# Kernel tuning notes

Measured on AMD Instinct MI355X. Metric: run time of the kernel, lower is better.

The kernel has to match this reference:

```python
import jax, jax.numpy as jnp
import numpy as np

N = 8192
F_IN = 128
N_META = 128
N_EMBED = 128


def setup_inputs() -> dict:
    key = jax.random.key(0)
    k1, k2, k3, k4, k5, k6 = jax.random.split(key, 6)
    X = jax.random.normal(k1, (N, F_IN), dtype=jnp.float32)
    A = jax.random.uniform(k2, (N, N), dtype=jnp.float32)  # dense nonneg adjacency
    s = 1.0 / np.sqrt(F_IN)
    W_embed = jax.random.uniform(k3, (N_EMBED, F_IN), dtype=jnp.float32, minval=-s, maxval=s)
    b_embed = jax.random.uniform(k4, (N_EMBED,), dtype=jnp.float32, minval=-s, maxval=s)
    W_assign = jax.random.uniform(k5, (N_META, F_IN), dtype=jnp.float32, minval=-s, maxval=s)
    b_assign = jax.random.uniform(k6, (N_META,), dtype=jnp.float32, minval=-s, maxval=s)
    return {"X": X, "A": A, "W_embed": W_embed, "b_embed": b_embed,
            "W_assign": W_assign, "b_assign": b_assign}


def reference(X, A, W_embed, b_embed, W_assign, b_assign):
    n = A.shape[0]
    # A_hat = A + I; symmetric normalization D^-1/2 A_hat D^-1/2.
    # (Original builds full diag matrices; result equals row/col scaling.)
    A_hat = A + jnp.eye(n, dtype=A.dtype)
    deg = jnp.sum(A_hat, axis=1)
    d_inv_sqrt = jnp.where(deg > 0, jax.lax.rsqrt(deg), 0.0)
    A_norm = d_inv_sqrt[:, None] * A_hat * d_inv_sqrt[None, :]
    AX = A_norm @ X  # shared by both GCN layers: [N, F]
    z_l = AX @ W_embed.T + b_embed                      # [N, n_embed]
    s_l = jax.nn.softmax(AX @ W_assign.T + b_assign, axis=-1)  # [N, n_meta]
    X_next = s_l.T @ z_l                                 # [n_meta, n_embed]
    A_next = s_l.T @ (A @ s_l)                           # [n_meta, n_meta]
    return (X_next, A_next, s_l)
```

## Files before the change

### kernel.cpp

```cpp
#include <hip/hip_runtime.h>
#include <hip/hip_bf16.h>
#include <cstdint>

typedef short v8s __attribute__((ext_vector_type(8)));
typedef float v4f __attribute__((ext_vector_type(4)));

#define DEV __device__ __forceinline__

DEV unsigned short f2bu(float f) {
  unsigned u = __builtin_bit_cast(unsigned, f);
  u += 0x7fffu + ((u >> 16) & 1u);
  return (unsigned short)(u >> 16);
}

DEV v8s pack8(const float4& a, const float4& b) {
  v8s r;
  r[0] = (short)f2bu(a.x); r[1] = (short)f2bu(a.y);
  r[2] = (short)f2bu(a.z); r[3] = (short)f2bu(a.w);
  r[4] = (short)f2bu(b.x); r[5] = (short)f2bu(b.y);
  r[6] = (short)f2bu(b.z); r[7] = (short)f2bu(b.w);
  return r;
}

DEV void gload16(const unsigned short* g, char* l) {
  __builtin_amdgcn_global_load_lds(
      (const __attribute__((address_space(1))) void*)g,
      (__attribute__((address_space(3))) void*)l, 16, 0, 0);
}

template<bool CVT>
__global__ __launch_bounds__(256)
void k_degcvt(const float* __restrict__ A, float* __restrict__ dinv,
              unsigned short* __restrict__ Abf) {
  const int row = blockIdx.x;
  const float* ar = A + (size_t)row * 8192;
  unsigned short* aw = Abf + (size_t)row * 8192;
  float s = 0.f;
  #pragma unroll
  for (int i = 0; i < 8; ++i) {
    const int c = i * 1024 + threadIdx.x * 4;
    float4 v = *(const float4*)(ar + c);
    s += (v.x + v.y) + (v.z + v.w);
    if constexpr (CVT) {
      uint2 w;
      w.x = (unsigned)f2bu(v.x) | ((unsigned)f2bu(v.y) << 16);
      w.y = (unsigned)f2bu(v.z) | ((unsigned)f2bu(v.w) << 16);
      *(uint2*)(aw + c) = w;
    }
  }
  #pragma unroll
  for (int d = 1; d < 64; d <<= 1) s += __shfl_xor(s, d);
  __shared__ float wsum[4];
  if ((threadIdx.x & 63) == 0) wsum[threadIdx.x >> 6] = s;
  __syncthreads();
  if (threadIdx.x == 0) {
    dinv[row] = rsqrtf(1.0f + ((wsum[0] + wsum[1]) + (wsum[2] + wsum[3])));
  }
}

template<bool SCALE>
__global__ __launch_bounds__(256)
void k_transpose(const float* __restrict__ in, unsigned short* __restrict__ out,
                 const float* __restrict__ dinv) {
  __shared__ float tile[32][129];
  const int j0 = blockIdx.x * 32;
  const int t = threadIdx.x;
  const int r0 = t >> 5, sl = t & 31;
  #pragma unroll
  for (int i = 0; i < 4; ++i) {
    int r = r0 + i * 8;
    float4 v = *(const float4*)(in + (size_t)(j0 + r) * 128 + sl * 4);
    float sc = 1.0f;
    if constexpr (SCALE) sc = dinv[j0 + r];
    tile[r][sl * 4 + 0] = v.x * sc;
    tile[r][sl * 4 + 1] = v.y * sc;
    tile[r][sl * 4 + 2] = v.z * sc;
    tile[r][sl * 4 + 3] = v.w * sc;
  }
  __syncthreads();
  const int c = t >> 1, h = t & 1;
  unsigned short* op = out + (size_t)c * 8192 + j0 + h * 16;
  #pragma unroll
  for (int q = 0; q < 2; ++q) {
    int rb = h * 16 + q * 8;
    uint4 w;
    w.x = (unsigned)f2bu(tile[rb + 0][c]) | ((unsigned)f2bu(tile[rb + 1][c]) << 16);
    w.y = (unsigned)f2bu(tile[rb + 2][c]) | ((unsigned)f2bu(tile[rb + 3][c]) << 16);
    w.z = (unsigned)f2bu(tile[rb + 4][c]) | ((unsigned)f2bu(tile[rb + 5][c]) << 16);
    w.w = (unsigned)f2bu(tile[rb + 6][c]) | ((unsigned)f2bu(tile[rb + 7][c]) << 16);
    *(uint4*)(op + q * 8) = w;
  }
}

__global__ __launch_bounds__(256, 4)
void k_gemm_v2(const unsigned short* __restrict__ Ab16,
               const unsigned short* __restrict__ Bt,
               float* __restrict__ parts) {
  __shared__ alignas(16) char bsm[2][16384];
  const int t = threadIdx.x;
  const int wv = t >> 6, l = t & 63;
  const int wr = wv >> 1, wcol = wv & 1;
  const int i0 = blockIdx.x * 64 + wr * 32;
  const int k0 = blockIdx.y * 1024;
  const int lr = l & 15, lq = l >> 4;

  const unsigned short* pA0 = Ab16 + (size_t)(i0 + lr) * 8192 + k0 + lq * 8;
  const unsigned short* pA1 = pA0 + (size_t)16 * 8192;

  const int swz = (l & 7) ^ ((l >> 3) & 7);
  const unsigned short* pS[4];
  #pragma unroll
  for (int i = 0; i < 4; ++i) {
    const int col = wv * 32 + i * 8 + (l >> 3);
    pS[i] = Bt + (size_t)col * 8192 + k0 + swz * 8;
  }

  v4f acc[2][4];
  #pragma unroll
  for (int mt = 0; mt < 2; ++mt)
    #pragma unroll
    for (int nt = 0; nt < 4; ++nt) acc[mt][nt] = (v4f){0.f, 0.f, 0.f, 0.f};

  v8s areg[2][2][2];

  auto stage = [&](int c, int buf) {
    #pragma unroll
    for (int i = 0; i < 4; ++i)
      gload16(pS[i] + c * 64, bsm[buf] + wv * 4096 + i * 1024);
  };
  auto loadA = [&](int c, int buf) {
    #pragma unroll
    for (int kf = 0; kf < 2; ++kf) {
      areg[buf][kf][0] = *(const v8s*)(pA0 + c * 64 + kf * 32);
      areg[buf][kf][1] = *(const v8s*)(pA1 + c * 64 + kf * 32);
    }
  };

  stage(0, 0);
  loadA(0, 0);
  __syncthreads();

  #pragma unroll
  for (int c = 0; c < 16; ++c) {
    if (c < 15) {
      stage(c + 1, (c + 1) & 1);
      loadA(c + 1, (c + 1) & 1);
    }
    #pragma unroll
    for (int kf = 0; kf < 2; ++kf) {
      #pragma unroll
      for (int nt = 0; nt < 4; ++nt) {
        const int col = wcol * 64 + nt * 16 + lr;
        const int off = ((col << 7) + kf * 64 + lq * 16) ^ ((col & 7) << 4);
        v8s bf = *(const v8s*)(bsm[c & 1] + off);
        acc[0][nt] = __builtin_amdgcn_mfma_f32_16x16x32_bf16(areg[c & 1][kf][0], bf, acc[0][nt], 0, 0, 0);
        acc[1][nt] = __builtin_amdgcn_mfma_f32_16x16x32_bf16(areg[c & 1][kf][1], bf, acc[1][nt], 0, 0, 0);
      }
    }
    if (c < 15) __syncthreads();
  }

  float* p = parts + (size_t)blockIdx.y * (8192 * 128);
  const int colb = wcol * 64;
  #pragma unroll
  for (int mt = 0; mt < 2; ++mt)
    #pragma unroll
    for (int nt = 0; nt < 4; ++nt)
      #pragma unroll
      for (int r = 0; r < 4; ++r)
        p[(size_t)(i0 + mt * 16 + lq * 4 + r) * 128 + colb + nt * 16 + lr] = acc[mt][nt][r];
}

__global__ __launch_bounds__(512)
void k_gemm_f32(const float* __restrict__ Af, const unsigned short* __restrict__ Bt,
                float* __restrict__ parts) {
  constexpr int KSTEPS = 2048 / 32;
  const int t = threadIdx.x;
  const int wv = t >> 6, l = t & 63;
  const int rg = wv >> 1, ch = wv & 1;
  const int i0 = blockIdx.x * 128 + rg * 32;
  const int k0 = blockIdx.y * 2048;
  const int lr = l & 15, lk = (l >> 4) * 8;

  const float* pAf0 = Af + (size_t)(i0 + lr) * 8192 + k0 + lk;
  const float* pAf1 = pAf0 + (size_t)16 * 8192;
  const unsigned short* pB[4];
  #pragma unroll
  for (int nt = 0; nt < 4; ++nt)
    pB[nt] = Bt + (size_t)(ch * 64 + nt * 16 + lr) * 8192 + k0 + lk;

  v4f acc[2][4];
  #pragma unroll
  for (int mt = 0; mt < 2; ++mt)
    #pragma unroll
    for (int nt = 0; nt < 4; ++nt) acc[mt][nt] = (v4f){0.f, 0.f, 0.f, 0.f};

  float4 af_[2][2][2];
  v8s bb[2][4];

  auto loadab = [&](int buf, int k) {
    af_[buf][0][0] = *(const float4*)(pAf0 + k);
    af_[buf][0][1] = *(const float4*)(pAf0 + k + 4);
    af_[buf][1][0] = *(const float4*)(pAf1 + k);
    af_[buf][1][1] = *(const float4*)(pAf1 + k + 4);
    #pragma unroll
    for (int nt = 0; nt < 4; ++nt) bb[buf][nt] = *(const v8s*)(pB[nt] + k);
  };
  auto mfmas = [&](int buf) {
    #pragma unroll
    for (int mt = 0; mt < 2; ++mt) {
      v8s a_ = pack8(af_[buf][mt][0], af_[buf][mt][1]);
      #pragma unroll
      for (int nt = 0; nt < 4; ++nt)
        acc[mt][nt] = __builtin_amdgcn_mfma_f32_16x16x32_bf16(a_, bb[buf][nt], acc[mt][nt], 0, 0, 0);
    }
  };

  loadab(0, 0);
  for (int kt = 0; kt < KSTEPS; kt += 2) {
    loadab(1, (kt + 1) * 32);
    mfmas(0);
    if (kt + 2 < KSTEPS) loadab(0, (kt + 2) * 32);
    mfmas(1);
  }

  float* p = parts + (size_t)blockIdx.y * (8192 * 128);
  const int colb = ch * 64;
  #pragma unroll
  for (int mt = 0; mt < 2; ++mt)
    #pragma unroll
    for (int nt = 0; nt < 4; ++nt)
      #pragma unroll
      for (int r = 0; r < 4; ++r)
        p[(size_t)(i0 + mt * 16 + (l >> 4) * 4 + r) * 128 + colb + nt * 16 + lr] = acc[mt][nt][r];
}

__global__ __launch_bounds__(256)
void k_post1(const float* __restrict__ parts, int nsplit,
             const float* __restrict__ dinv, const float* __restrict__ Xg,
             const float* __restrict__ We, const float* __restrict__ be,
             const float* __restrict__ Wa, const float* __restrict__ ba,
             float* __restrict__ sl_out, unsigned short* __restrict__ slt,
             unsigned short* __restrict__ zlt) {
  __shared__ alignas(16) unsigned short axs[32 * 128];
  __shared__ float lg[32 * 128];
  __shared__ unsigned short sbf[32 * 130];
  __shared__ unsigned short zbf[32 * 130];
  const int t = threadIdx.x;
  const int i0 = blockIdx.x * 32;

  {
    const int r = t >> 3, cg = t & 7;
    const size_t base = (size_t)(i0 + r) * 128 + cg * 16;
    float acc[16];
    #pragma unroll
    for (int q = 0; q < 4; ++q) {
      float4 v = *(const float4*)(parts + base + q * 4);
      acc[q * 4 + 0] = v.x; acc[q * 4 + 1] = v.y;
      acc[q * 4 + 2] = v.z; acc[q * 4 + 3] = v.w;
    }
    for (int s = 1; s < nsplit; ++s) {
      #pragma unroll
      for (int q = 0; q < 4; ++q) {
        float4 v = *(const float4*)(parts + (size_t)s * 1048576 + base + q * 4);
        acc[q * 4 + 0] += v.x; acc[q * 4 + 1] += v.y;
        acc[q * 4 + 2] += v.z; acc[q * 4 + 3] += v.w;
      }
    }
    const float di = dinv[i0 + r];
    unsigned short bx[16];
    #pragma unroll
    for (int q = 0; q < 4; ++q) {
      float4 xv = *(const float4*)(Xg + base + q * 4);
      bx[q * 4 + 0] = f2bu(di * (acc[q * 4 + 0] + di * xv.x));
      bx[q * 4 + 1] = f2bu(di * (acc[q * 4 + 1] + di * xv.y));
      bx[q * 4 + 2] = f2bu(di * (acc[q * 4 + 2] + di * xv.z));
      bx[q * 4 + 3] = f2bu(di * (acc[q * 4 + 3] + di * xv.w));
    }
    char* Ab = (char*)axs;
    const int b0 = (r << 8) + cg * 32, sw = (r & 7) << 4;
    uint4 w0, w1;
    w0.x = (unsigned)bx[0] | ((unsigned)bx[1] << 16);
    w0.y = (unsigned)bx[2] | ((unsigned)bx[3] << 16);
    w0.z = (unsigned)bx[4] | ((unsigned)bx[5] << 16);
    w0.w = (unsigned)bx[6] | ((unsigned)bx[7] << 16);
    w1.x = (unsigned)bx[8] | ((unsigned)bx[9] << 16);
    w1.y = (unsigned)bx[10] | ((unsigned)bx[11] << 16);
    w1.z = (unsigned)bx[12] | ((unsigned)bx[13] << 16);
    w1.w = (unsigned)bx[14] | ((unsigned)bx[15] << 16);
    *(uint4*)(Ab + (b0 ^ sw)) = w0;
    *(uint4*)(Ab + ((b0 + 16) ^ sw)) = w1;
  }
  __syncthreads();

  const int wv = t >> 6, l = t & 63, fr = l & 15;
  {
    v4f zac[2][2], lac[2][2];
    #pragma unroll
    for (int a = 0; a < 2; ++a)
      #pragma unroll
      for (int b = 0; b < 2; ++b) {
        zac[a][b] = (v4f){0.f, 0.f, 0.f, 0.f};
        lac[a][b] = (v4f){0.f, 0.f, 0.f, 0.f};
      }
    const int kk = (l >> 4) * 8;
    #pragma unroll
    for (int ks = 0; ks < 4; ++ks) {
      const int k = ks * 32 + kk;
      #pragma unroll
      for (int nj = 0; nj < 2; ++nj) {
        const int col = nj * 64 + wv * 16 + fr;
        v8s bfe = pack8(*(const float4*)(We + col * 128 + k),
                        *(const float4*)(We + col * 128 + k + 4));
        v8s bfa = pack8(*(const float4*)(Wa + col * 128 + k),
                        *(const float4*)(Wa + col * 128 + k + 4));
        #pragma unroll
        for (int mt = 0; mt < 2; ++mt) {
          const int arow = mt * 16 + fr;
          v8s af = *(const v8s*)((char*)axs + (((arow << 8) + k * 2) ^ ((fr & 7) << 4)));
          zac[mt][nj] = __builtin_amdgcn_mfma_f32_16x16x32_bf16(af, bfe, zac[mt][nj], 0, 0, 0);
          lac[mt][nj] = __builtin_amdgcn_mfma_f32_16x16x32_bf16(af, bfa, lac[mt][nj], 0, 0, 0);
        }
      }
    }
    #pragma unroll
    for (int mt = 0; mt < 2; ++mt)
      #pragma unroll
      for (int nj = 0; nj < 2; ++nj)
        #pragma unroll
        for (int r4 = 0; r4 < 4; ++r4) {
          const int row = mt * 16 + (l >> 4) * 4 + r4;
          const int col = nj * 64 + wv * 16 + fr;
          lg[row * 128 + col] = lac[mt][nj][r4] + ba[col];
          zbf[row * 130 + col] = f2bu(zac[mt][nj][r4] + be[col]);
        }
  }
  __syncthreads();

  {
    const int r = t >> 3, g = t & 7;
    const float* lp = lg + r * 128 + g * 16;
    float x[16];
    #pragma unroll
    for (int q = 0; q < 4; ++q) {
      float4 v = *(const float4*)(lp + q * 4);
      x[q * 4 + 0] = v.x; x[q * 4 + 1] = v.y; x[q * 4 + 2] = v.z; x[q * 4 + 3] = v.w;
    }
    float mx = x[0];
    #pragma unroll
    for (int j = 1; j < 16; ++j) mx = fmaxf(mx, x[j]);
    #pragma unroll
    for (int d = 1; d < 8; d <<= 1) mx = fmaxf(mx, __shfl_xor(mx, d));
    float sum = 0.f;
    #pragma unroll
    for (int j = 0; j < 16; ++j) { x[j] = __expf(x[j] - mx); sum += x[j]; }
    #pragma unroll
    for (int d = 1; d < 8; d <<= 1) sum += __shfl_xor(sum, d);
    const float inv = 1.0f / sum;
    float* op = sl_out + (size_t)(i0 + r) * 128 + g * 16;
    #pragma unroll
    for (int q = 0; q < 4; ++q) {
      float4 o;
      o.x = x[q * 4 + 0] * inv; o.y = x[q * 4 + 1] * inv;
      o.z = x[q * 4 + 2] * inv; o.w = x[q * 4 + 3] * inv;
      *(float4*)(op + q * 4) = o;
    }
    #pragma unroll
    for (int j = 0; j < 16; ++j) sbf[r * 130 + g * 16 + j] = f2bu(x[j] * inv);
  }
  __syncthreads();

  {
    const int c = t & 127;
    const unsigned short* src = (t < 128) ? sbf : zbf;
    unsigned short* dst = (t < 128) ? slt : zlt;
    unsigned short* o = dst + (size_t)c * 8192 + i0;
    #pragma unroll
    for (int q = 0; q < 4; ++q) {
      uint4 w;
      w.x = (unsigned)src[(q * 8 + 0) * 130 + c] | ((unsigned)src[(q * 8 + 1) * 130 + c] << 16);
      w.y = (unsigned)src[(q * 8 + 2) * 130 + c] | ((unsigned)src[(q * 8 + 3) * 130 + c] << 16);
      w.z = (unsigned)src[(q * 8 + 4) * 130 + c] | ((unsigned)src[(q * 8 + 5) * 130 + c] << 16);
      w.w = (unsigned)src[(q * 8 + 6) * 130 + c] | ((unsigned)src[(q * 8 + 7) * 130 + c] << 16);
      *(uint4*)(o + q * 8) = w;
    }
  }
}

__global__ __launch_bounds__(256)
void k_post2(const float* __restrict__ parts, int nsplit, unsigned short* __restrict__ ast) {
  __shared__ unsigned short sb[32 * 130];
  const int t = threadIdx.x;
  const int i0 = blockIdx.x * 32;
  {
    const int r = t >> 3, cg = t & 7;
    const size_t base = (size_t)(i0 + r) * 128 + cg * 16;
    float acc[16];
    #pragma unroll
    for (int q = 0; q < 4; ++q) {
      float4 v = *(const float4*)(parts + base + q * 4);
      acc[q * 4 + 0] = v.x; acc[q * 4 + 1] = v.y;
      acc[q * 4 + 2] = v.z; acc[q * 4 + 3] = v.w;
    }
    for (int s = 1; s < nsplit; ++s) {
      #pragma unroll
      for (int q = 0; q < 4; ++q) {
        float4 v = *(const float4*)(parts + (size_t)s * 1048576 + base + q * 4);
        acc[q * 4 + 0] += v.x; acc[q * 4 + 1] += v.y;
        acc[q * 4 + 2] += v.z; acc[q * 4 + 3] += v.w;
      }
    }
    #pragma unroll
    for (int j = 0; j < 16; ++j) sb[r * 130 + cg * 16 + j] = f2bu(acc[j]);
  }
  __syncthreads();
  if (t < 128) {
    unsigned short* o = ast + (size_t)t * 8192 + i0;
    #pragma unroll
    for (int q = 0; q < 4; ++q) {
      uint4 w;
      w.x = (unsigned)sb[(q * 8 + 0) * 130 + t] | ((unsigned)sb[(q * 8 + 1) * 130 + t] << 16);
      w.y = (unsigned)sb[(q * 8 + 2) * 130 + t] | ((unsigned)sb[(q * 8 + 3) * 130 + t] << 16);
      w.z = (unsigned)sb[(q * 8 + 4) * 130 + t] | ((unsigned)sb[(q * 8 + 5) * 130 + t] << 16);
      w.w = (unsigned)sb[(q * 8 + 6) * 130 + t] | ((unsigned)sb[(q * 8 + 7) * 130 + t] << 16);
      *(uint4*)(o + q * 8) = w;
    }
  }
}

__global__ __launch_bounds__(256)
void k_outer(const unsigned short* __restrict__ slt, const unsigned short* __restrict__ zlt,
             const unsigned short* __restrict__ ast, float* __restrict__ parts) {
  const int t = threadIdx.x, wv = t >> 6, ln = t & 63;
  const int k0 = blockIdx.x * 128;
  const int lm = ln & 15, lk = (ln >> 4) << 3;
  v4f c1[2][8];
  v4f c2[2][8];
  #pragma unroll
  for (int mt = 0; mt < 2; ++mt)
    #pragma unroll
    for (int nt = 0; nt < 8; ++nt) { c1[mt][nt] = (v4f){0.f,0.f,0.f,0.f}; c2[mt][nt] = (v4f){0.f,0.f,0.f,0.f}; }
  #pragma unroll
  for (int ks = 0; ks < 4; ++ks) {
    int k = k0 + ks * 32 + lk;
    v8s a0 = *(const v8s*)(slt + (size_t)(wv * 32 + lm) * 8192 + k);
    v8s a1 = *(const v8s*)(slt + (size_t)(wv * 32 + 16 + lm) * 8192 + k);
    #pragma unroll
    for (int nt = 0; nt < 8; ++nt) {
      v8s bz = *(const v8s*)(zlt + (size_t)(nt * 16 + lm) * 8192 + k);
      v8s bs = *(const v8s*)(ast + (size_t)(nt * 16 + lm) * 8192 + k);
      c1[0][nt] = __builtin_amdgcn_mfma_f32_16x16x32_bf16(a0, bz, c1[0][nt], 0, 0, 0);
      c1[1][nt] = __builtin_amdgcn_mfma_f32_16x16x32_bf16(a1, bz, c1[1][nt], 0, 0, 0);
      c2[0][nt] = __builtin_amdgcn_mfma_f32_16x16x32_bf16(a0, bs, c2[0][nt], 0, 0, 0);
      c2[1][nt] = __builtin_amdgcn_mfma_f32_16x16x32_bf16(a1, bs, c2[1][nt], 0, 0, 0);
    }
  }
  float* p = parts + (size_t)blockIdx.x * 32768;
  #pragma unroll
  for (int mt = 0; mt < 2; ++mt)
    #pragma unroll
    for (int nt = 0; nt < 8; ++nt)
      #pragma unroll
      for (int r = 0; r < 4; ++r) {
        int m = wv * 32 + mt * 16 + ((ln >> 4) << 2) + r;
        int n = nt * 16 + lm;
        p[m * 128 + n] = c1[mt][nt][r];
        p[16384 + m * 128 + n] = c2[mt][nt][r];
      }
}

__global__ __launch_bounds__(256)
void k_reduce(const float* __restrict__ parts, float* __restrict__ out) {
  const int o = blockIdx.x * 256 + threadIdx.x;
  float s = 0.f;
  for (int b = 0; b < 64; ++b) s += parts[(size_t)b * 32768 + o];
  out[o] = s;
}

extern "C" void kernel_launch(void* const* d_in, const int* in_sizes, int n_in,
                              void* d_out, int out_size, void* d_ws, size_t ws_size,
                              hipStream_t stream) {
  (void)in_sizes; (void)n_in; (void)out_size;
  const float* X  = (const float*)d_in[0];
  const float* A  = (const float*)d_in[1];
  const float* We = (const float*)d_in[2];
  const float* be = (const float*)d_in[3];
  const float* Wa = (const float*)d_in[4];
  const float* ba = (const float*)d_in[5];
  float* out = (float*)d_out;
  float* sl = out + 32768;

  char* ws = (char*)d_ws;
  constexpr size_t OFF_XPT  = 32768;
  constexpr size_t OFF_SLT  = OFF_XPT + 2097152;
  constexpr size_t OFF_ZLT  = OFF_SLT + 2097152;
  constexpr size_t OFF_AST  = OFF_ZLT + 2097152;
  constexpr size_t OFF_PART = OFF_AST + 2097152;
  constexpr size_t OFF_ABF  = OFF_PART + 67108864;
  constexpr size_t NEED_ABF = OFF_ABF + 134217728ull;

  float*          dinv = (float*)(ws + 0);
  unsigned short* xpt  = (unsigned short*)(ws + OFF_XPT);
  unsigned short* slt  = (unsigned short*)(ws + OFF_SLT);
  unsigned short* zlt  = (unsigned short*)(ws + OFF_ZLT);
  unsigned short* ast  = (unsigned short*)(ws + OFF_AST);
  float*          part = (float*)(ws + OFF_PART);
  unsigned short* abfp = (unsigned short*)(ws + OFF_ABF);

  const bool abf = ws_size >= NEED_ABF;
  const int  sk  = abf ? 8 : 4;

  if (abf) k_degcvt<true><<<8192, 256, 0, stream>>>(A, dinv, abfp);
  else     k_degcvt<false><<<8192, 256, 0, stream>>>(A, dinv, abfp);

  k_transpose<true><<<256, 256, 0, stream>>>(X, xpt, dinv);

  if (abf) k_gemm_v2<<<dim3(128, 8), 256, 0, stream>>>(abfp, xpt, part);
  else     k_gemm_f32<<<dim3(64, 4), 512, 0, stream>>>(A, xpt, part);

  k_post1<<<256, 256, 0, stream>>>(part, sk, dinv, X, We, be, Wa, ba, sl, slt, zlt);

  if (abf) k_gemm_v2<<<dim3(128, 8), 256, 0, stream>>>(abfp, slt, part);
  else     k_gemm_f32<<<dim3(64, 4), 512, 0, stream>>>(A, slt, part);

  k_post2<<<256, 256, 0, stream>>>(part, sk, ast);
  k_outer<<<64, 256, 0, stream>>>(slt, zlt, ast, part);
  k_reduce<<<128, 256, 0, stream>>>(part, out);
}
```

Measured before the change: 219.4 us.

## Read fp32 A directly in GEMMs and drop the bf16 copy of A

Removes the pre-pass that wrote a bf16 copy of the 8192x8192 adjacency matrix. The LDS-staged GEMM now loads fp32 A rows directly and converts them to bf16 in registers before each MFMA, using a per-k-fragment double-buffered register prefetch. This removes the 128MB bf16 write and the workspace-size fallback path. In exchange, each of the two GEMM passes reads twice as many A bytes, and the conversion arithmetic now sits in the inner loop.

```diff
diff --git a/kernel.cpp b/kernel.cpp
--- a/kernel.cpp
+++ b/kernel.cpp
@@ -28,25 +28,15 @@
       (__attribute__((address_space(3))) void*)l, 16, 0, 0);
 }
 
-template<bool CVT>
-__global__ __launch_bounds__(256)
-void k_degcvt(const float* __restrict__ A, float* __restrict__ dinv,
-              unsigned short* __restrict__ Abf) {
+__global__ __launch_bounds__(256)
+void k_deg(const float* __restrict__ A, float* __restrict__ dinv) {
   const int row = blockIdx.x;
   const float* ar = A + (size_t)row * 8192;
-  unsigned short* aw = Abf + (size_t)row * 8192;
   float s = 0.f;
   #pragma unroll
   for (int i = 0; i < 8; ++i) {
-    const int c = i * 1024 + threadIdx.x * 4;
-    float4 v = *(const float4*)(ar + c);
+    float4 v = *(const float4*)(ar + i * 1024 + threadIdx.x * 4);
     s += (v.x + v.y) + (v.z + v.w);
-    if constexpr (CVT) {
-      uint2 w;
-      w.x = (unsigned)f2bu(v.x) | ((unsigned)f2bu(v.y) << 16);
-      w.y = (unsigned)f2bu(v.z) | ((unsigned)f2bu(v.w) << 16);
-      *(uint2*)(aw + c) = w;
-    }
   }
   #pragma unroll
   for (int d = 1; d < 64; d <<= 1) s += __shfl_xor(s, d);
@@ -93,7 +83,7 @@
 }
 
 __global__ __launch_bounds__(256, 4)
-void k_gemm_v2(const unsigned short* __restrict__ Ab16,
+void k_gemm_v3(const float* __restrict__ Af,
                const unsigned short* __restrict__ Bt,
                float* __restrict__ parts) {
   __shared__ alignas(16) char bsm[2][16384];
@@ -104,8 +94,8 @@
   const int k0 = blockIdx.y * 1024;
   const int lr = l & 15, lq = l >> 4;
 
-  const unsigned short* pA0 = Ab16 + (size_t)(i0 + lr) * 8192 + k0 + lq * 8;
-  const unsigned short* pA1 = pA0 + (size_t)16 * 8192;
+  const float* pAf0 = Af + (size_t)(i0 + lr) * 8192 + k0 + lq * 8;
+  const float* pAf1 = pAf0 + (size_t)16 * 8192;
 
   const int swz = (l & 7) ^ ((l >> 3) & 7);
   const unsigned short* pS[4];
@@ -121,19 +111,18 @@
     #pragma unroll
     for (int nt = 0; nt < 4; ++nt) acc[mt][nt] = (v4f){0.f, 0.f, 0.f, 0.f};
 
-  v8s areg[2][2][2];
+  float4 af[2][2][2];
 
   auto stage = [&](int c, int buf) {
     #pragma unroll
     for (int i = 0; i < 4; ++i)
       gload16(pS[i] + c * 64, bsm[buf] + wv * 4096 + i * 1024);
   };
-  auto loadA = [&](int c, int buf) {
-    #pragma unroll
-    for (int kf = 0; kf < 2; ++kf) {
-      areg[buf][kf][0] = *(const v8s*)(pA0 + c * 64 + kf * 32);
-      areg[buf][kf][1] = *(const v8s*)(pA1 + c * 64 + kf * 32);
-    }
+  auto loadA = [&](int kfi, int buf) {
+    af[buf][0][0] = *(const float4*)(pAf0 + kfi * 32);
+    af[buf][0][1] = *(const float4*)(pAf0 + kfi * 32 + 4);
+    af[buf][1][0] = *(const float4*)(pAf1 + kfi * 32);
+    af[buf][1][1] = *(const float4*)(pAf1 + kfi * 32 + 4);
   };
 
   stage(0, 0);
@@ -142,19 +131,20 @@
 
   #pragma unroll
   for (int c = 0; c < 16; ++c) {
-    if (c < 15) {
-      stage(c + 1, (c + 1) & 1);
-      loadA(c + 1, (c + 1) & 1);
-    }
+    if (c < 15) stage(c + 1, (c + 1) & 1);
     #pragma unroll
     for (int kf = 0; kf < 2; ++kf) {
+      const int kfi = c * 2 + kf;
+      if (kfi + 1 < 32) loadA(kfi + 1, (kfi + 1) & 1);
+      v8s a0 = pack8(af[kfi & 1][0][0], af[kfi & 1][0][1]);
+      v8s a1 = pack8(af[kfi & 1][1][0], af[kfi & 1][1][1]);
       #pragma unroll
       for (int nt = 0; nt < 4; ++nt) {
         const int col = wcol * 64 + nt * 16 + lr;
         const int off = ((col << 7) + kf * 64 + lq * 16) ^ ((col & 7) << 4);
         v8s bf = *(const v8s*)(bsm[c & 1] + off);
-        acc[0][nt] = __builtin_amdgcn_mfma_f32_16x16x32_bf16(areg[c & 1][kf][0], bf, acc[0][nt], 0, 0, 0);
-        acc[1][nt] = __builtin_amdgcn_mfma_f32_16x16x32_bf16(areg[c & 1][kf][1], bf, acc[1][nt], 0, 0, 0);
+        acc[0][nt] = __builtin_amdgcn_mfma_f32_16x16x32_bf16(a0, bf, acc[0][nt], 0, 0, 0);
+        acc[1][nt] = __builtin_amdgcn_mfma_f32_16x16x32_bf16(a1, bf, acc[1][nt], 0, 0, 0);
       }
     }
     if (c < 15) __syncthreads();
@@ -169,70 +159,6 @@
       #pragma unroll
       for (int r = 0; r < 4; ++r)
         p[(size_t)(i0 + mt * 16 + lq * 4 + r) * 128 + colb + nt * 16 + lr] = acc[mt][nt][r];
-}
-
-__global__ __launch_bounds__(512)
-void k_gemm_f32(const float* __restrict__ Af, const unsigned short* __restrict__ Bt,
-                float* __restrict__ parts) {
-  constexpr int KSTEPS = 2048 / 32;
-  const int t = threadIdx.x;
-  const int wv = t >> 6, l = t & 63;
-  const int rg = wv >> 1, ch = wv & 1;
-  const int i0 = blockIdx.x * 128 + rg * 32;
-  const int k0 = blockIdx.y * 2048;
-  const int lr = l & 15, lk = (l >> 4) * 8;
-
-  const float* pAf0 = Af + (size_t)(i0 + lr) * 8192 + k0 + lk;
-  const float* pAf1 = pAf0 + (size_t)16 * 8192;
-  const unsigned short* pB[4];
-  #pragma unroll
-  for (int nt = 0; nt < 4; ++nt)
-    pB[nt] = Bt + (size_t)(ch * 64 + nt * 16 + lr) * 8192 + k0 + lk;
-
-  v4f acc[2][4];
-  #pragma unroll
-  for (int mt = 0; mt < 2; ++mt)
-    #pragma unroll
-    for (int nt = 0; nt < 4; ++nt) acc[mt][nt] = (v4f){0.f, 0.f, 0.f, 0.f};
-
-  float4 af_[2][2][2];
-  v8s bb[2][4];
-
-  auto loadab = [&](int buf, int k) {
-    af_[buf][0][0] = *(const float4*)(pAf0 + k);
-    af_[buf][0][1] = *(const float4*)(pAf0 + k + 4);
-    af_[buf][1][0] = *(const float4*)(pAf1 + k);
-    af_[buf][1][1] = *(const float4*)(pAf1 + k + 4);
-    #pragma unroll
-    for (int nt = 0; nt < 4; ++nt) bb[buf][nt] = *(const v8s*)(pB[nt] + k);
-  };
-  auto mfmas = [&](int buf) {
-    #pragma unroll
-    for (int mt = 0; mt < 2; ++mt) {
-      v8s a_ = pack8(af_[buf][mt][0], af_[buf][mt][1]);
-      #pragma unroll
-      for (int nt = 0; nt < 4; ++nt)
-        acc[mt][nt] = __builtin_amdgcn_mfma_f32_16x16x32_bf16(a_, bb[buf][nt], acc[mt][nt], 0, 0, 0);
-    }
-  };
-
-  loadab(0, 0);
-  for (int kt = 0; kt < KSTEPS; kt += 2) {
-    loadab(1, (kt + 1) * 32);
-    mfmas(0);
-    if (kt + 2 < KSTEPS) loadab(0, (kt + 2) * 32);
-    mfmas(1);
-  }
-
-  float* p = parts + (size_t)blockIdx.y * (8192 * 128);
-  const int colb = ch * 64;
-  #pragma unroll
-  for (int mt = 0; mt < 2; ++mt)
-    #pragma unroll
-    for (int nt = 0; nt < 4; ++nt)
-      #pragma unroll
-      for (int r = 0; r < 4; ++r)
-        p[(size_t)(i0 + mt * 16 + (l >> 4) * 4 + r) * 128 + colb + nt * 16 + lr] = acc[mt][nt][r];
 }
 
 __global__ __launch_bounds__(256)
@@ -480,7 +406,7 @@
 extern "C" void kernel_launch(void* const* d_in, const int* in_sizes, int n_in,
                               void* d_out, int out_size, void* d_ws, size_t ws_size,
                               hipStream_t stream) {
-  (void)in_sizes; (void)n_in; (void)out_size;
+  (void)in_sizes; (void)n_in; (void)out_size; (void)ws_size;
   const float* X  = (const float*)d_in[0];
   const float* A  = (const float*)d_in[1];
   const float* We = (const float*)d_in[2];
@@ -496,8 +422,6 @@
   constexpr size_t OFF_ZLT  = OFF_SLT + 2097152;
   constexpr size_t OFF_AST  = OFF_ZLT + 2097152;
   constexpr size_t OFF_PART = OFF_AST + 2097152;
-  constexpr size_t OFF_ABF  = OFF_PART + 67108864;
-  constexpr size_t NEED_ABF = OFF_ABF + 134217728ull;
 
   float*          dinv = (float*)(ws + 0);
   unsigned short* xpt  = (unsigned short*)(ws + OFF_XPT);
@@ -505,25 +429,13 @@
   unsigned short* zlt  = (unsigned short*)(ws + OFF_ZLT);
   unsigned short* ast  = (unsigned short*)(ws + OFF_AST);
   float*          part = (float*)(ws + OFF_PART);
-  unsigned short* abfp = (unsigned short*)(ws + OFF_ABF);
-
-  const bool abf = ws_size >= NEED_ABF;
-  const int  sk  = abf ? 8 : 4;
-
-  if (abf) k_degcvt<true><<<8192, 256, 0, stream>>>(A, dinv, abfp);
-  else     k_degcvt<false><<<8192, 256, 0, stream>>>(A, dinv, abfp);
-
+
+  k_deg<<<8192, 256, 0, stream>>>(A, dinv);
   k_transpose<true><<<256, 256, 0, stream>>>(X, xpt, dinv);
-
-  if (abf) k_gemm_v2<<<dim3(128, 8), 256, 0, stream>>>(abfp, xpt, part);
-  else     k_gemm_f32<<<dim3(64, 4), 512, 0, stream>>>(A, xpt, part);
-
-  k_post1<<<256, 256, 0, stream>>>(part, sk, dinv, X, We, be, Wa, ba, sl, slt, zlt);
-
-  if (abf) k_gemm_v2<<<dim3(128, 8), 256, 0, stream>>>(abfp, slt, part);
-  else     k_gemm_f32<<<dim3(64, 4), 512, 0, stream>>>(A, slt, part);
-
-  k_post2<<<256, 256, 0, stream>>>(part, sk, ast);
+  k_gemm_v3<<<dim3(128, 8), 256, 0, stream>>>(A, xpt, part);
+  k_post1<<<256, 256, 0, stream>>>(part, 8, dinv, X, We, be, Wa, ba, sl, slt, zlt);
+  k_gemm_v3<<<dim3(128, 8), 256, 0, stream>>>(A, slt, part);
+  k_post2<<<256, 256, 0, stream>>>(part, 8, ast);
   k_outer<<<64, 256, 0, stream>>>(slt, zlt, ast, part);
   k_reduce<<<128, 256, 0, stream>>>(part, out);
 }
```

Result: slower. 257.9 us (+17.6%).
